# Optimization experiments

Hardware: AMD Instinct MI355X
Metric: run time of the kernel (lower is better)

Reference implementation:

```python
import jax, jax.numpy as jnp
import numpy as np

ALPHA = 0.2  # LeakyReLU negative slope
NEG_BIG = -9e15

def setup_inputs() -> dict:
    key = jax.random.key(0)
    k1, k2, k3, k4 = jax.random.split(key, 4)
    N, F_in, F_out = 8192, 512, 64
    inp = jax.random.normal(k1, (N, F_in), dtype=jnp.float32)
    adj = jax.random.randint(k2, (N, N), 0, 2, dtype=jnp.int32)
    W = jax.random.normal(k3, (F_in, F_out), dtype=jnp.float32) * (1.414 / np.sqrt(F_in + F_out))
    a = jax.random.normal(k4, (2 * F_out, 1), dtype=jnp.float32) * 0.1
    return {"input": inp, "adj": adj, "W": W, "a": a}

def reference(input, adj, W, a):
    # h: [N, F_out]
    h = input @ W
    F_out = h.shape[1]
    # Decompose a into a1 (source part) and a2 (target part):
    a1 = a[:F_out, 0]   # [F_out]
    a2 = a[F_out:, 0]   # [F_out]
    s1 = h @ a1         # [N]
    s2 = h @ a2         # [N]
    e = s1[:, None] + s2[None, :]                      # [N, N]
    e = jnp.where(e > 0, e, ALPHA * e)                 # LeakyReLU
    e = jnp.where(adj > 0, e, jnp.float32(NEG_BIG))    # mask non-edges
    attention = jax.nn.softmax(e, axis=1)              # [N, N]
    # dropout with p=0.0 / eval mode -> identity
    h_prime = attention @ h                            # [N, F_out]
    return h_prime
```

## Files before the change

kernel.cpp:

```cpp
#include <hip/hip_runtime.h>
#include <hip/hip_bf16.h>

#define ALPHA 0.2f

constexpr int N    = 8192;
constexpr int FIN  = 512;
constexpr int FOUT = 64;
constexpr int NSPLIT = 16;
constexpr int JCHUNK = N / NSPLIT;
constexpr int NB     = N / 8;

typedef __attribute__((ext_vector_type(8))) short short8;
typedef __attribute__((ext_vector_type(4))) float f32x4;

__global__ __launch_bounds__(256) void k0_pack(const int* __restrict__ adj,
                                               unsigned char* __restrict__ bits)
{
    const int lane = threadIdx.x & 63;
    const int wv   = threadIdx.x >> 6;
    const int g    = blockIdx.x * 4 + wv;
    const int i    = g >> 2;
    const int segb = (g & 3) * 4;
    const int* row = adj + (size_t)i * N;

    int4 va[8];
    #pragma unroll
    for (int u = 0; u < 4; ++u) {
        const int jb = (segb + u) * 512 + lane * 8;
        va[2 * u]     = *(const int4*)(row + jb);
        va[2 * u + 1] = *(const int4*)(row + jb + 4);
    }
    #pragma unroll
    for (int u = 0; u < 4; ++u) {
        const int4 a = va[2 * u], b = va[2 * u + 1];
        unsigned int byte =
            (a.x != 0 ?   1u : 0u) | (a.y != 0 ?   2u : 0u) |
            (a.z != 0 ?   4u : 0u) | (a.w != 0 ?   8u : 0u) |
            (b.x != 0 ?  16u : 0u) | (b.y != 0 ?  32u : 0u) |
            (b.z != 0 ?  64u : 0u) | (b.w != 0 ? 128u : 0u);
        bits[(size_t)i * NB + (segb + u) * 64 + lane] = (unsigned char)byte;
    }
}

__global__ __launch_bounds__(256) void k1_proj(
    const float* __restrict__ input, const float* __restrict__ W,
    const float* __restrict__ a, __hip_bfloat16* __restrict__ hbT,
    float* __restrict__ s1, float* __restrict__ s2)
{
    __shared__ __hip_bfloat16 tile[8][64];
    const int tid  = threadIdx.x;
    const int col  = tid & 63;
    const int g    = tid >> 6;
    const int rbase = blockIdx.x * 8;

    float acc[2] = {0.f, 0.f};
    const float* in0 = input + (size_t)(rbase + g * 2) * FIN;

    for (int k = 0; k < FIN; k += 8) {
        float w[8];
        #pragma unroll
        for (int q = 0; q < 8; ++q) w[q] = W[(k + q) * FOUT + col];
        const float4 x0a = *(const float4*)(in0 + 0 * FIN + k);
        const float4 x0b = *(const float4*)(in0 + 0 * FIN + k + 4);
        const float4 x1a = *(const float4*)(in0 + 1 * FIN + k);
        const float4 x1b = *(const float4*)(in0 + 1 * FIN + k + 4);
        acc[0] = fmaf(x0a.w, w[3], fmaf(x0a.z, w[2], fmaf(x0a.y, w[1], fmaf(x0a.x, w[0], acc[0]))));
        acc[0] = fmaf(x0b.w, w[7], fmaf(x0b.z, w[6], fmaf(x0b.y, w[5], fmaf(x0b.x, w[4], acc[0]))));
        acc[1] = fmaf(x1a.w, w[3], fmaf(x1a.z, w[2], fmaf(x1a.y, w[1], fmaf(x1a.x, w[0], acc[1]))));
        acc[1] = fmaf(x1b.w, w[7], fmaf(x1b.z, w[6], fmaf(x1b.y, w[5], fmaf(x1b.x, w[4], acc[1]))));
    }

    const float a1c = a[col];
    const float a2c = a[FOUT + col];
    #pragma unroll
    for (int q = 0; q < 2; ++q) {
        float r1 = acc[q] * a1c;
        float r2 = acc[q] * a2c;
        #pragma unroll
        for (int off = 32; off >= 1; off >>= 1) {
            r1 += __shfl_xor(r1, off, 64);
            r2 += __shfl_xor(r2, off, 64);
        }
        if (col == 0) {
            s1[rbase + g * 2 + q] = r1;
            s2[rbase + g * 2 + q] = r2;
        }
        tile[g * 2 + q][col] = __float2bfloat16(acc[q]);
    }
    __syncthreads();

    if (tid < 128) {
        const int c = tid >> 1, part = tid & 1;
        unsigned short v[4];
        #pragma unroll
        for (int u = 0; u < 4; ++u) {
            __hip_bfloat16 hv = tile[part * 4 + u][c];
            v[u] = *reinterpret_cast<unsigned short*>(&hv);
        }
        *(ushort4*)((unsigned short*)hbT + (size_t)c * N + rbase + part * 4) =
            make_ushort4(v[0], v[1], v[2], v[3]);
    }
}

__global__ __launch_bounds__(256, 4) void k2_attn(
    const unsigned char* __restrict__ bits,
    const float* __restrict__ s1, const float* __restrict__ s2,
    const unsigned short* __restrict__ hbT,
    float* __restrict__ pAcc, float* __restrict__ pZ)
{
    const int r   = blockIdx.x;
    const int s   = blockIdx.y;
    const int tid = threadIdx.x;
    const int w    = tid >> 6;
    const int lane = tid & 63;
    const int row16 = lane & 15;
    const int quad  = lane >> 4;

    const int i = r * 64 + w * 16 + row16;
    const float s1i = s1[i];
    const int jbeg = s * JCHUNK;
    const int jend = jbeg + JCHUNK;

    f32x4 acc0 = {0.f, 0.f, 0.f, 0.f};
    f32x4 acc1 = {0.f, 0.f, 0.f, 0.f};
    f32x4 acc2 = {0.f, 0.f, 0.f, 0.f};
    f32x4 acc3 = {0.f, 0.f, 0.f, 0.f};
    float zpart = 0.f;

    const unsigned char* brow = bits + (size_t)i * NB;
    const short* hp = (const short*)hbT;

    unsigned int cM = *(const unsigned int*)(brow + (jbeg >> 3));
    float4 cSa = *(const float4*)(s2 + jbeg + quad * 8);
    float4 cSb = *(const float4*)(s2 + jbeg + quad * 8 + 4);

    for (int j0 = jbeg; j0 < jend; j0 += 32) {
        const int j0n = (j0 + 32 < jend) ? (j0 + 32) : jbeg;
        const unsigned int nM = *(const unsigned int*)(brow + (j0n >> 3));
        const float4 nSa = *(const float4*)(s2 + j0n + quad * 8);
        const float4 nSb = *(const float4*)(s2 + j0n + quad * 8 + 4);

        const int jj = j0 + quad * 8;
        const short8 b0 = *(const short8*)(hp + (size_t)(row16 +  0) * N + jj);
        const short8 b1 = *(const short8*)(hp + (size_t)(row16 + 16) * N + jj);
        const short8 b2 = *(const short8*)(hp + (size_t)(row16 + 32) * N + jj);
        const short8 b3 = *(const short8*)(hp + (size_t)(row16 + 48) * N + jj);

        const unsigned int mbyte = (cM >> (8 * quad)) & 0xffu;
        float s2v[8];
        s2v[0] = cSa.x; s2v[1] = cSa.y; s2v[2] = cSa.z; s2v[3] = cSa.w;
        s2v[4] = cSb.x; s2v[5] = cSb.y; s2v[6] = cSb.z; s2v[7] = cSb.w;

        short8 afrag;
        #pragma unroll
        for (int j = 0; j < 8; ++j) {
            float e = s1i + s2v[j];
            e = fmaxf(e, ALPHA * e);
            float pv = __expf(e);
            pv = ((mbyte >> j) & 1u) ? pv : 0.f;
            __hip_bfloat16 hv = __float2bfloat16(pv);
            zpart += __bfloat162float(hv);
            afrag[j] = *reinterpret_cast<short*>(&hv);
        }

        acc0 = __builtin_amdgcn_mfma_f32_16x16x32_bf16(afrag, b0, acc0, 0, 0, 0);
        acc1 = __builtin_amdgcn_mfma_f32_16x16x32_bf16(afrag, b1, acc1, 0, 0, 0);
        acc2 = __builtin_amdgcn_mfma_f32_16x16x32_bf16(afrag, b2, acc2, 0, 0, 0);
        acc3 = __builtin_amdgcn_mfma_f32_16x16x32_bf16(afrag, b3, acc3, 0, 0, 0);

        cM = nM; cSa = nSa; cSb = nSb;
    }

    zpart += __shfl_xor(zpart, 16, 64);
    zpart += __shfl_xor(zpart, 32, 64);
    if (quad == 0) pZ[(size_t)s * N + i] = zpart;

    float* outp = pAcc + ((size_t)s * N + (size_t)r * 64 + w * 16) * FOUT;
    #pragma unroll
    for (int reg = 0; reg < 4; ++reg) {
        const int row = quad * 4 + reg;
        outp[row * FOUT + ( 0 + row16)] = acc0[reg];
        outp[row * FOUT + (16 + row16)] = acc1[reg];
        outp[row * FOUT + (32 + row16)] = acc2[reg];
        outp[row * FOUT + (48 + row16)] = acc3[reg];
    }
}

__global__ __launch_bounds__(256) void k3_combine(
    const float* __restrict__ pAcc, const float* __restrict__ pZ,
    float* __restrict__ out)
{
    const int idx = blockIdx.x * 256 + threadIdx.x;
    const int i = idx >> 6;
    float num = 0.f, den = 0.f;
    #pragma unroll
    for (int s = 0; s < NSPLIT; ++s) {
        num += pAcc[(size_t)s * N * FOUT + idx];
        den += pZ[(size_t)s * N + i];
    }
    out[idx] = num / den;
}

extern "C" void kernel_launch(void* const* d_in, const int* in_sizes, int n_in,
                              void* d_out, int out_size, void* d_ws, size_t ws_size,
                              hipStream_t stream)
{
    const float* input = (const float*)d_in[0];
    const int*   adj   = (const int*)d_in[1];
    const float* W     = (const float*)d_in[2];
    const float* a     = (const float*)d_in[3];
    float* out = (float*)d_out;

    char* ws = (char*)d_ws;
    __hip_bfloat16* hbT = (__hip_bfloat16*)ws;
    float* s1   = (float*)(ws + (size_t)FOUT * N * 2);
    float* s2   = s1 + N;
    float* pZ   = s2 + N;
    float* pAcc = pZ + (size_t)NSPLIT * N;
    unsigned char* bitsP = (unsigned char*)(pAcc + (size_t)NSPLIT * N * FOUT);

    k0_pack<<<8192, 256, 0, stream>>>(adj, bitsP);
    k1_proj<<<N / 8, 256, 0, stream>>>(input, W, a, hbT, s1, s2);

    dim3 g2(N / 64, NSPLIT);
    k2_attn<<<g2, 256, 0, stream>>>(bitsP, s1, s2, (const unsigned short*)hbT, pAcc, pZ);

    k3_combine<<<(N * FOUT) / 256, 256, 0, stream>>>(pAcc, pZ, out);
}
```

Before: 512.8 us.

## Stage hT, mask and s2 chunk in LDS and double the j-split

The attention kernel now cooperatively loads the block's bf16 h^T slice (64 x JCHUNK, padded rows), the packed mask words for its 64 rows, and the s2 chunk into shared memory, then runs a fully unrolled MFMA loop reading from LDS. Previously each of the four waves re-fetched the same h^T tiles from global/L2. NSPLIT doubles to 32, halving each chunk so the tile fits in LDS and giving more blocks. The cost is more partial sums to write and combine, about 34KB of LDS per block that may limit occupancy, and a barrier before compute with no overlap of the load phase.

```diff
diff --git a/kernel.cpp b/kernel.cpp
--- a/kernel.cpp
+++ b/kernel.cpp
@@ -6,9 +6,10 @@
 constexpr int N    = 8192;
 constexpr int FIN  = 512;
 constexpr int FOUT = 64;
-constexpr int NSPLIT = 16;
+constexpr int NSPLIT = 32;
 constexpr int JCHUNK = N / NSPLIT;
 constexpr int NB     = N / 8;
+constexpr int LROW   = JCHUNK + 8;
 
 typedef __attribute__((ext_vector_type(8))) short short8;
 typedef __attribute__((ext_vector_type(4))) float f32x4;
@@ -108,18 +109,39 @@
     const unsigned short* __restrict__ hbT,
     float* __restrict__ pAcc, float* __restrict__ pZ)
 {
+    __shared__ unsigned short Bl[64 * LROW];
+    __shared__ unsigned int   Ml[64 * 9];
+    __shared__ float          S2l[JCHUNK];
+
     const int r   = blockIdx.x;
     const int s   = blockIdx.y;
     const int tid = threadIdx.x;
-    const int w    = tid >> 6;
-    const int lane = tid & 63;
+    const int w     = tid >> 6;
+    const int lane  = tid & 63;
     const int row16 = lane & 15;
     const int quad  = lane >> 4;
-
-    const int i = r * 64 + w * 16 + row16;
+    const int jbeg  = s * JCHUNK;
+
+    #pragma unroll
+    for (int rr = 0; rr < 8; ++rr) {
+        const int seg = rr * 256 + tid;
+        const int f = seg >> 5, o = seg & 31;
+        const short8 v = *(const short8*)((const short*)hbT + (size_t)f * N + jbeg + o * 8);
+        *(short8*)(&Bl[f * LROW + o * 8]) = v;
+    }
+    #pragma unroll
+    for (int rr = 0; rr < 2; ++rr) {
+        const int idx = rr * 256 + tid;
+        const int row = idx >> 3, col = idx & 7;
+        Ml[row * 9 + col] =
+            *(const unsigned int*)(bits + (size_t)(r * 64 + row) * NB + (jbeg >> 3) + col * 4);
+    }
+    S2l[tid] = s2[jbeg + tid];
+    __syncthreads();
+
+    const int iloc = w * 16 + row16;
+    const int i    = r * 64 + iloc;
     const float s1i = s1[i];
-    const int jbeg = s * JCHUNK;
-    const int jend = jbeg + JCHUNK;
 
     f32x4 acc0 = {0.f, 0.f, 0.f, 0.f};
     f32x4 acc1 = {0.f, 0.f, 0.f, 0.f};
@@ -127,29 +149,25 @@
     f32x4 acc3 = {0.f, 0.f, 0.f, 0.f};
     float zpart = 0.f;
 
-    const unsigned char* brow = bits + (size_t)i * NB;
-    const short* hp = (const short*)hbT;
-
-    unsigned int cM = *(const unsigned int*)(brow + (jbeg >> 3));
-    float4 cSa = *(const float4*)(s2 + jbeg + quad * 8);
-    float4 cSb = *(const float4*)(s2 + jbeg + quad * 8 + 4);
-
-    for (int j0 = jbeg; j0 < jend; j0 += 32) {
-        const int j0n = (j0 + 32 < jend) ? (j0 + 32) : jbeg;
-        const unsigned int nM = *(const unsigned int*)(brow + (j0n >> 3));
-        const float4 nSa = *(const float4*)(s2 + j0n + quad * 8);
-        const float4 nSb = *(const float4*)(s2 + j0n + quad * 8 + 4);
-
-        const int jj = j0 + quad * 8;
-        const short8 b0 = *(const short8*)(hp + (size_t)(row16 +  0) * N + jj);
-        const short8 b1 = *(const short8*)(hp + (size_t)(row16 + 16) * N + jj);
-        const short8 b2 = *(const short8*)(hp + (size_t)(row16 + 32) * N + jj);
-        const short8 b3 = *(const short8*)(hp + (size_t)(row16 + 48) * N + jj);
-
+    #pragma unroll
+    for (int it = 0; it < JCHUNK / 32; ++it) {
+        const int j0rel = it * 32;
+        const int jj    = j0rel + quad * 8;
+
+        const unsigned int cM    = Ml[iloc * 9 + it];
         const unsigned int mbyte = (cM >> (8 * quad)) & 0xffu;
+
+        const float4 sA = *(const float4*)(&S2l[jj]);
+        const float4 sB = *(const float4*)(&S2l[jj + 4]);
+
+        const short8 b0 = *(const short8*)(&Bl[(row16 +  0) * LROW + jj]);
+        const short8 b1 = *(const short8*)(&Bl[(row16 + 16) * LROW + jj]);
+        const short8 b2 = *(const short8*)(&Bl[(row16 + 32) * LROW + jj]);
+        const short8 b3 = *(const short8*)(&Bl[(row16 + 48) * LROW + jj]);
+
         float s2v[8];
-        s2v[0] = cSa.x; s2v[1] = cSa.y; s2v[2] = cSa.z; s2v[3] = cSa.w;
-        s2v[4] = cSb.x; s2v[5] = cSb.y; s2v[6] = cSb.z; s2v[7] = cSb.w;
+        s2v[0] = sA.x; s2v[1] = sA.y; s2v[2] = sA.z; s2v[3] = sA.w;
+        s2v[4] = sB.x; s2v[5] = sB.y; s2v[6] = sB.z; s2v[7] = sB.w;
 
         short8 afrag;
         #pragma unroll
@@ -167,8 +185,6 @@
         acc1 = __builtin_amdgcn_mfma_f32_16x16x32_bf16(afrag, b1, acc1, 0, 0, 0);
         acc2 = __builtin_amdgcn_mfma_f32_16x16x32_bf16(afrag, b2, acc2, 0, 0, 0);
         acc3 = __builtin_amdgcn_mfma_f32_16x16x32_bf16(afrag, b3, acc3, 0, 0, 0);
-
-        cM = nM; cSa = nSa; cSb = nSb;
     }
 
     zpart += __shfl_xor(zpart, 16, 64);
```

Measured after the change: 471.0 us. -8.1%, faster.
